# Kernel optimization log

Hardware: AMD Instinct MI355X
Metric: run time of the kernel (lower is better)

## Reference

```python
import jax, jax.numpy as jnp
import numpy as np

N, E, H, OUT, L = 50000, 500000, 256, 128, 2
EPS = 1e-5  # torch LayerNorm default


def _make_edges(k):
    # both rows cover all N nodes so that unique()/remap in the original is identity
    k1, k2, kp = jax.random.split(k, 3)
    row0 = jnp.concatenate([jax.random.permutation(kp, N), jax.random.randint(k1, (E - N,), 0, N)])
    row1 = jnp.concatenate([jnp.arange(N), jax.random.randint(k2, (E - N,), 0, N)])
    return jnp.stack([row0, row1]).astype(jnp.int32)


def setup_inputs() -> dict:
    key = jax.random.key(0)
    ks = jax.random.split(key, 7)
    s = 0.02
    x = jax.random.normal(ks[0], (N, H), jnp.float32)
    edge_r1 = _make_edges(ks[1])
    edge_r2 = _make_edges(ks[2])
    Wl = jax.random.normal(ks[3], (L, H, H), jnp.float32) * s
    W0 = jax.random.normal(ks[4], (L, H, H), jnp.float32) * s
    W1 = jax.random.normal(ks[5], (L, H, H), jnp.float32) * s
    bl = jnp.zeros((L, H), jnp.float32)
    b0 = jnp.zeros((L, H), jnp.float32)
    b1 = jnp.zeros((L, H), jnp.float32)
    gamma = jnp.ones((L, H), jnp.float32)
    beta = jnp.zeros((L, H), jnp.float32)
    Wout = jax.random.normal(ks[6], (OUT, H), jnp.float32) * s
    bout = jnp.zeros((OUT,), jnp.float32)
    return dict(x=x, edge_r1=edge_r1, edge_r2=edge_r2, Wl=Wl, bl=bl, W0=W0, b0=b0,
                W1=W1, b1=b1, gamma=gamma, beta=beta, Wout=Wout, bout=bout)


def _layer(i, h, x0, e, Wl, bl, W0, b0, W1, b1, gamma, beta):
    # PyG flow='target_to_source', aggr='add': gather h at e[1], scatter-add at e[0]
    agg = jax.ops.segment_sum(h[e[1]], e[0], num_segments=h.shape[0])  # [N, H]
    z = agg @ Wl[i].T + bl[i] + h @ W0[i].T + b0[i] + x0 @ W1[i].T + b1[i]
    z = jax.nn.relu(z)
    mu = jnp.mean(z, axis=-1, keepdims=True)
    var = jnp.mean(jnp.square(z - mu), axis=-1, keepdims=True)
    return (z - mu) * jax.lax.rsqrt(var + EPS) * gamma[i] + beta[i]  # dropout is identity in eval


def reference(x, edge_r1, edge_r2, Wl, bl, W0, b0, W1, b1, gamma, beta, Wout, bout):
    # reversed(metapath): (C,r2,C) with conv_idx=1 first, then (C,r1,C) with conv_idx=0
    h = _layer(1, x, x, edge_r2, Wl, bl, W0, b0, W1, b1, gamma, beta)
    h = _layer(0, h, x, edge_r1, Wl, bl, W0, b0, W1, b1, gamma, beta)
    return h @ Wout.T + bout  # [N, OUT]
```

## Files before the change

kernel.cpp:

```cpp
#include <hip/hip_runtime.h>
#include <stdint.h>

#define N_NODES 50000
#define N_EDGES 500000
#define NPAD    50048
#define NB      196
#define EPS     1e-5f

typedef _Float16 half8_ __attribute__((ext_vector_type(8)));
typedef _Float16 half4_ __attribute__((ext_vector_type(4)));
typedef float    float4_ __attribute__((ext_vector_type(4)));

typedef uint32_t u32_g __attribute__((address_space(1)));
typedef uint32_t u32_s __attribute__((address_space(3)));

__device__ __forceinline__ void gload16(const void* g, void* lds_wave_base) {
    __builtin_amdgcn_global_load_lds((const u32_g*)g, (u32_s*)lds_wave_base, 16, 0, 0);
}

__global__ void count_rank_kernel(const int* __restrict__ e1, const int* __restrict__ e2,
                                  int* __restrict__ cnt, int* __restrict__ ranks,
                                  int e, int n) {
    const int set = blockIdx.y;
    const int* dst = set ? e2 : e1;
    int* c = cnt + set * n;
    int* r = ranks + set * e;
    int i0 = (blockIdx.x * 256 + threadIdx.x) * 8;
    if (i0 >= e) return;
    int4 d0 = *(const int4*)(dst + i0);
    int4 d1 = *(const int4*)(dst + i0 + 4);
    int r0 = atomicAdd(&c[d0.x], 1);
    int r1 = atomicAdd(&c[d0.y], 1);
    int r2 = atomicAdd(&c[d0.z], 1);
    int r3 = atomicAdd(&c[d0.w], 1);
    int r4 = atomicAdd(&c[d1.x], 1);
    int r5 = atomicAdd(&c[d1.y], 1);
    int r6 = atomicAdd(&c[d1.z], 1);
    int r7 = atomicAdd(&c[d1.w], 1);
    *(int4*)(r + i0)     = make_int4(r0, r1, r2, r3);
    *(int4*)(r + i0 + 4) = make_int4(r4, r5, r6, r7);
}

__global__ void bsum_kernel(const int* __restrict__ cnt, int* __restrict__ bsums, int n) {
    const int* c = cnt + blockIdx.y * n;
    int i = blockIdx.x * 256 + threadIdx.x;
    int v = (i < n) ? c[i] : 0;
    for (int off = 32; off > 0; off >>= 1) v += __shfl_xor(v, off, 64);
    __shared__ int ws[4];
    if ((threadIdx.x & 63) == 0) ws[threadIdx.x >> 6] = v;
    __syncthreads();
    if (threadIdx.x == 0)
        bsums[blockIdx.y * 256 + blockIdx.x] = ws[0] + ws[1] + ws[2] + ws[3];
}

__global__ void bscan_kernel(int* __restrict__ bsums, int* __restrict__ rp1,
                             int* __restrict__ rp2, int nb, int n) {
    __shared__ int sm[512];
    int t = threadIdx.x;
    int idx = t & 255;
    int v = (idx < nb) ? bsums[t] : 0;
    sm[t] = v;
    __syncthreads();
    for (int off = 1; off < 256; off <<= 1) {
        int x = sm[t];
        if (idx >= off) x += sm[t - off];
        __syncthreads();
        sm[t] = x;
        __syncthreads();
    }
    if (idx < nb) bsums[t] = (idx > 0) ? sm[t - 1] : 0;
    if (t == 255)  rp1[n] = sm[255];
    if (t == 511)  rp2[n] = sm[511];
}

__global__ void bscatter_kernel(const int* __restrict__ cnt, const int* __restrict__ bsums,
                                int* __restrict__ rp, int n) {
    const int* c = cnt + blockIdx.y * n;
    int* rpS = rp + blockIdx.y * (n + 1);
    __shared__ int sm[256];
    int t = threadIdx.x;
    int i = blockIdx.x * 256 + t;
    int v = (i < n) ? c[i] : 0;
    sm[t] = v;
    __syncthreads();
    for (int off = 1; off < 256; off <<= 1) {
        int x = sm[t];
        if (t >= off) x += sm[t - off];
        __syncthreads();
        sm[t] = x;
        __syncthreads();
    }
    int excl = sm[t] - v + bsums[blockIdx.y * 256 + blockIdx.x];
    if (i < n) rpS[i] = excl;
}

__global__ void place_kernel(const int* __restrict__ e1, const int* __restrict__ e2,
                             const int* __restrict__ ranks, const int* __restrict__ rp,
                             int* __restrict__ col, int e, int n) {
    const int set = blockIdx.y;
    const int* ed = set ? e2 : e1;
    const int* r  = ranks + set * e;
    const int* rpS = rp + set * (n + 1);
    int* cl = col + set * e;
    int i0 = (blockIdx.x * 256 + threadIdx.x) * 8;
    if (i0 >= e) return;
    int4 d0 = *(const int4*)(ed + i0);
    int4 d1 = *(const int4*)(ed + i0 + 4);
    int4 s0 = *(const int4*)(ed + e + i0);
    int4 s1 = *(const int4*)(ed + e + i0 + 4);
    int4 k0 = *(const int4*)(r + i0);
    int4 k1 = *(const int4*)(r + i0 + 4);
    int p0 = rpS[d0.x] + k0.x;
    int p1 = rpS[d0.y] + k0.y;
    int p2 = rpS[d0.z] + k0.z;
    int p3 = rpS[d0.w] + k0.w;
    int p4 = rpS[d1.x] + k1.x;
    int p5 = rpS[d1.y] + k1.y;
    int p6 = rpS[d1.z] + k1.z;
    int p7 = rpS[d1.w] + k1.w;
    cl[p0] = s0.x; cl[p1] = s0.y; cl[p2] = s0.z; cl[p3] = s0.w;
    cl[p4] = s1.x; cl[p5] = s1.y; cl[p6] = s1.z; cl[p7] = s1.w;
}

__global__ void copyx_kernel(const float* __restrict__ x, _Float16* __restrict__ xh, int n) {
    int i = blockIdx.x * 256 + threadIdx.x;
    if (i >= n * 64) return;
    float4_ v = ((const float4_*)x)[i];
    half4_ h;
    h[0] = (_Float16)v[0]; h[1] = (_Float16)v[1];
    h[2] = (_Float16)v[2]; h[3] = (_Float16)v[3];
    ((half4_*)xh)[i] = h;
}

__global__ void pad_kernel(_Float16* __restrict__ a, _Float16* __restrict__ b,
                           _Float16* __restrict__ c, _Float16* __restrict__ d) {
    int i = blockIdx.x * 256 + threadIdx.x;
    int buf = i / 3072, j = i % 3072;
    _Float16* p = (buf == 0) ? a : (buf == 1) ? b : (buf == 2) ? c : d;
    half4_ z = {(_Float16)0.f, (_Float16)0.f, (_Float16)0.f, (_Float16)0.f};
    *(half4_*)(p + (size_t)N_NODES * 256 + (size_t)j * 4) = z;
}

__global__ void wcat_kernel(const float* __restrict__ Wl, const float* __restrict__ W0,
                            const float* __restrict__ W1, const float* __restrict__ Wout,
                            _Float16* __restrict__ Wcat) {
    int i = blockIdx.x * 256 + threadIdx.x;
    if (i < 2 * 256 * 768) {
        int l = i / (256 * 768);
        int r = i % (256 * 768);
        int j = r / 768, k = r % 768;
        const float* s = (k < 256) ? Wl : (k < 512 ? W0 : W1);
        Wcat[i] = (_Float16)s[l * 65536 + j * 256 + (k & 255)];
    } else if (i < 2 * 256 * 768 + 128 * 256) {
        int r = i - 2 * 256 * 768;
        Wcat[i] = (_Float16)Wout[r];
    }
}

__global__ void bias_kernel(const float* __restrict__ bl, const float* __restrict__ b0,
                            const float* __restrict__ b1, const float* __restrict__ bout,
                            float* __restrict__ bias) {
    int i = blockIdx.x * 256 + threadIdx.x;
    if (i < 512)       bias[i] = bl[i] + b0[i] + b1[i];
    else if (i < 640)  bias[i] = bout[i - 512];
}

__global__ void gather_kernel(const _Float16* __restrict__ hin,
                              const int* __restrict__ rowptr, const int* __restrict__ col,
                              _Float16* __restrict__ dst, int n) {
    int node = blockIdx.x * 4 + (threadIdx.x >> 6);
    int lane = threadIdx.x & 63;
    int half = lane >> 5, l5 = lane & 31;
    if (node >= n) return;
    int s = rowptr[node], e = rowptr[node + 1];
    float a[8] = {0.f, 0.f, 0.f, 0.f, 0.f, 0.f, 0.f, 0.f};
    float b[8] = {0.f, 0.f, 0.f, 0.f, 0.f, 0.f, 0.f, 0.f};
    int i = s + half;
    for (; i + 2 < e; i += 4) {
        int c0 = col[i], c1 = col[i + 2];
        half8_ v0 = *(const half8_*)(hin + (size_t)c0 * 256 + l5 * 8);
        half8_ v1 = *(const half8_*)(hin + (size_t)c1 * 256 + l5 * 8);
#pragma unroll
        for (int j = 0; j < 8; j++) { a[j] += (float)v0[j]; b[j] += (float)v1[j]; }
    }
    for (; i < e; i += 2) {
        int c0 = col[i];
        half8_ v0 = *(const half8_*)(hin + (size_t)c0 * 256 + l5 * 8);
#pragma unroll
        for (int j = 0; j < 8; j++) a[j] += (float)v0[j];
    }
    half8_ o;
#pragma unroll
    for (int j = 0; j < 8; j++) {
        float t = a[j] + b[j];
        t += __shfl_xor(t, 32, 64);
        o[j] = (_Float16)t;
    }
    if (half == 0)
        *(half8_*)(dst + (size_t)node * 256 + l5 * 8) = o;
}

__global__ __launch_bounds__(512) void gemm_ln(const _Float16* __restrict__ agg,
                                               const _Float16* __restrict__ hsrc,
                                               const _Float16* __restrict__ xh,
                                               const _Float16* __restrict__ Bw,
                                               const float* __restrict__ bias,
                                               const float* __restrict__ gamma,
                                               const float* __restrict__ beta,
                                               _Float16* __restrict__ H) {
    __shared__ __align__(16) char smem[49152];
    char* AsB = smem;
    char* BsB = smem + 16384;
    const int rowBase = blockIdx.x * 128;
    const int tid  = threadIdx.x;
    const int lane = tid & 63;
    const int w    = tid >> 6;
    const int wm = w & 1, wn = w >> 1;
    const int quad = lane >> 4, mr = lane & 15;
    const int x7 = mr & 7;

    float4_ acc[4][4];
#pragma unroll
    for (int i = 0; i < 4; i++)
#pragma unroll
        for (int j = 0; j < 4; j++) { float4_ z4 = {0.f, 0.f, 0.f, 0.f}; acc[i][j] = z4; }

    int cA0 = w * 64 + lane, cA1 = cA0 + 512;
    int rA0 = cA0 >> 3, rA1 = cA1 >> 3;
    size_t offA0 = (size_t)(rowBase + rA0) * 256 + (((cA0 & 7) ^ (rA0 & 7)) * 8);
    size_t offA1 = (size_t)(rowBase + rA1) * 256 + (((cA1 & 7) ^ (rA1 & 7)) * 8);
    size_t offB[4];
#pragma unroll
    for (int j = 0; j < 4; j++) {
        int c = j * 512 + w * 64 + lane;
        int r = c >> 3;
        offB[j] = (size_t)r * 768 + (((c & 7) ^ (r & 7)) * 8);
    }
    void* lA0 = AsB + w * 1024;
    void* lA1 = AsB + 8192 + w * 1024;

    for (int k0 = 0; k0 < 768; k0 += 64) {
        const _Float16* src = (k0 < 256) ? agg : (k0 < 512) ? hsrc : xh;
        const int kloc = k0 & 255;
        gload16(src + offA0 + kloc, lA0);
        gload16(src + offA1 + kloc, lA1);
        gload16(Bw + offB[0] + k0, BsB + w * 1024);
        gload16(Bw + offB[1] + k0, BsB + 8192 + w * 1024);
        gload16(Bw + offB[2] + k0, BsB + 16384 + w * 1024);
        gload16(Bw + offB[3] + k0, BsB + 24576 + w * 1024);
        __syncthreads();
#pragma unroll
        for (int s = 0; s < 2; s++) {
            half8_ a[4], b[4];
#pragma unroll
            for (int im = 0; im < 4; im++) {
                int row = wm * 64 + im * 16 + mr;
                a[im] = *(const half8_*)(AsB + row * 128 + (((s * 4 + quad) ^ x7) * 16));
            }
#pragma unroll
            for (int in = 0; in < 4; in++) {
                int row = wn * 64 + in * 16 + mr;
                b[in] = *(const half8_*)(BsB + row * 128 + (((s * 4 + quad) ^ x7) * 16));
            }
#pragma unroll
            for (int im = 0; im < 4; im++)
#pragma unroll
                for (int in = 0; in < 4; in++)
                    acc[im][in] = __builtin_amdgcn_mfma_f32_16x16x32_f16(a[im], b[in], acc[im][in], 0, 0, 0);
        }
        __syncthreads();
    }

    float bv[4], gv[4], bev[4];
#pragma unroll
    for (int in = 0; in < 4; in++) {
        int colg = wn * 64 + in * 16 + mr;
        bv[in]  = bias[colg];
        gv[in]  = gamma[colg];
        bev[in] = beta[colg];
    }
    float* lnbuf   = (float*)AsB;
    float* lnstats = (float*)(AsB + 4096);

#pragma unroll
    for (int im = 0; im < 4; im++)
#pragma unroll
        for (int r = 0; r < 4; r++) {
            float s = 0.f, sq = 0.f;
#pragma unroll
            for (int in = 0; in < 4; in++) {
                float v = acc[im][in][r] + bv[in];
                v = v > 0.f ? v : 0.f;
                s += v; sq += v * v;
            }
            s  += __shfl_xor(s, 1, 64);  sq += __shfl_xor(sq, 1, 64);
            s  += __shfl_xor(s, 2, 64);  sq += __shfl_xor(sq, 2, 64);
            s  += __shfl_xor(s, 4, 64);  sq += __shfl_xor(sq, 4, 64);
            s  += __shfl_xor(s, 8, 64);  sq += __shfl_xor(sq, 8, 64);
            if (mr == 0) {
                int rl = wm * 64 + im * 16 + quad * 4 + r;
                lnbuf[(wn * 128 + rl) * 2]     = s;
                lnbuf[(wn * 128 + rl) * 2 + 1] = sq;
            }
        }
    __syncthreads();
    if (tid < 128) {
        float s  = lnbuf[tid * 2]             + lnbuf[(128 + tid) * 2]
                 + lnbuf[(256 + tid) * 2]     + lnbuf[(384 + tid) * 2];
        float sq = lnbuf[tid * 2 + 1]         + lnbuf[(128 + tid) * 2 + 1]
                 + lnbuf[(256 + tid) * 2 + 1] + lnbuf[(384 + tid) * 2 + 1];
        float mu  = s * (1.0f / 256.0f);
        float var = sq * (1.0f / 256.0f) - mu * mu;
        lnstats[tid * 2]     = mu;
        lnstats[tid * 2 + 1] = rsqrtf(var + EPS);
    }
    __syncthreads();

    _Float16* BsH = (_Float16*)BsB;
#pragma unroll
    for (int p = 0; p < 2; p++) {
        if (wm == p) {
#pragma unroll
            for (int im = 0; im < 4; im++)
#pragma unroll
                for (int r = 0; r < 4; r++) {
                    int rl = im * 16 + quad * 4 + r;
                    float mu = lnstats[(p * 64 + rl) * 2];
                    float rs = lnstats[(p * 64 + rl) * 2 + 1];
#pragma unroll
                    for (int in = 0; in < 4; in++) {
                        float v = acc[im][in][r] + bv[in];
                        v = v > 0.f ? v : 0.f;
                        BsH[rl * 256 + wn * 64 + in * 16 + mr] =
                            (_Float16)((v - mu) * rs * gv[in] + bev[in]);
                    }
                }
        }
        __syncthreads();
#pragma unroll
        for (int i = 0; i < 4; i++) {
            int c = i * 512 + tid;
            int row = c >> 5, ch = c & 31;
            half8_ v = *(const half8_*)(BsB + c * 16);
            *(half8_*)(H + (size_t)(rowBase + p * 64 + row) * 256 + ch * 8) = v;
        }
        __syncthreads();
    }
}

__global__ __launch_bounds__(256) void gemm_bt(const _Float16* __restrict__ A, int lda,
                                               const _Float16* __restrict__ B, int ldb,
                                               const float* __restrict__ bias,
                                               float* __restrict__ C, int ldc,
                                               int K, int Mstore) {
    __shared__ _Float16 As[128 * 32];
    __shared__ _Float16 Bs[128 * 32];
    const int rowBase = blockIdx.x * 128;
    const int colBase = blockIdx.y * 128;
    const int tid  = threadIdx.x;
    const int lane = tid & 63;
    const int w    = tid >> 6;
    const int wm = w & 1, wn = w >> 1;
    const int quad = lane >> 4, mr = lane & 15;

    float4_ acc[4][4];
#pragma unroll
    for (int i = 0; i < 4; i++)
#pragma unroll
        for (int j = 0; j < 4; j++) { float4_ z4 = {0.f, 0.f, 0.f, 0.f}; acc[i][j] = z4; }

    const int c0  = w * 64 + lane;
    const int rA0 = c0 >> 2;
    const int ko  = (c0 & 3) * 8;
    char* AsB = (char*)As;
    char* BsB = (char*)Bs;
    void* lA0 = AsB + w * 1024;
    void* lA1 = AsB + 4096 + w * 1024;
    void* lB0 = BsB + w * 1024;
    void* lB1 = BsB + 4096 + w * 1024;
    const _Float16* gA0 = A + (size_t)(rowBase + rA0) * lda + ko;
    const _Float16* gA1 = gA0 + (size_t)64 * lda;
    const _Float16* gB0 = B + (size_t)(colBase + rA0) * ldb + ko;
    const _Float16* gB1 = gB0 + (size_t)64 * ldb;

    for (int k0 = 0; k0 < K; k0 += 32) {
        gload16(gA0 + k0, lA0);
        gload16(gA1 + k0, lA1);
        gload16(gB0 + k0, lB0);
        gload16(gB1 + k0, lB1);
        __syncthreads();
        half8_ a[4], b[4];
#pragma unroll
        for (int im = 0; im < 4; im++)
            a[im] = *(const half8_*)(AsB + ((wm * 64 + im * 16 + mr) * 64 + quad * 16));
#pragma unroll
        for (int in = 0; in < 4; in++)
            b[in] = *(const half8_*)(BsB + ((wn * 64 + in * 16 + mr) * 64 + quad * 16));
#pragma unroll
        for (int im = 0; im < 4; im++)
#pragma unroll
            for (int in = 0; in < 4; in++)
                acc[im][in] = __builtin_amdgcn_mfma_f32_16x16x32_f16(a[im], b[in], acc[im][in], 0, 0, 0);
        __syncthreads();
    }

#pragma unroll
    for (int in = 0; in < 4; in++) {
        const int colg = colBase + wn * 64 + in * 16 + mr;
        const float bv = bias[colg];
#pragma unroll
        for (int im = 0; im < 4; im++) {
            float4_ c = acc[im][in];
#pragma unroll
            for (int r = 0; r < 4; r++) {
                int row = rowBase + wm * 64 + im * 16 + quad * 4 + r;
                if (row < Mstore) C[(size_t)row * ldc + colg] = c[r] + bv;
            }
        }
    }
}

extern "C" void kernel_launch(void* const* d_in, const int* in_sizes, int n_in,
                              void* d_out, int out_size, void* d_ws, size_t ws_size,
                              hipStream_t stream) {
    const float* x    = (const float*)d_in[0];
    const int*   e1   = (const int*)d_in[1];
    const int*   e2   = (const int*)d_in[2];
    const float* Wl   = (const float*)d_in[3];
    const float* bl   = (const float*)d_in[4];
    const float* W0   = (const float*)d_in[5];
    const float* b0   = (const float*)d_in[6];
    const float* W1   = (const float*)d_in[7];
    const float* b1   = (const float*)d_in[8];
    const float* gamma= (const float*)d_in[9];
    const float* beta = (const float*)d_in[10];
    const float* Wout = (const float*)d_in[11];
    const float* bout = (const float*)d_in[12];

    char* ws = (char*)d_ws;
    size_t off = 0;
    auto alloc = [&](size_t bytes) -> char* {
        char* p = ws + off;
        off = (off + bytes + 255) & ~(size_t)255;
        return p;
    };
    _Float16* xh   = (_Float16*)alloc((size_t)NPAD * 256 * 2);
    _Float16* aggb = (_Float16*)alloc((size_t)NPAD * 256 * 2);
    _Float16* h1   = (_Float16*)alloc((size_t)NPAD * 256 * 2);
    _Float16* h2   = (_Float16*)alloc((size_t)NPAD * 256 * 2);
    _Float16* Wcat = (_Float16*)alloc((size_t)(2 * 256 * 768 + 128 * 256) * 2);
    float*    bias = (float*)alloc(640 * 4);
    int* cnt   = (int*)alloc((size_t)2 * N_NODES * 4);
    int* rp    = (int*)alloc((size_t)2 * (N_NODES + 1) * 4);
    int* ranks = (int*)alloc((size_t)2 * N_EDGES * 4);
    int* col   = (int*)alloc((size_t)2 * N_EDGES * 4);
    int* bsums = (int*)alloc(512 * 4);

    int* rp1 = rp, *rp2 = rp + (N_NODES + 1);
    int* col1 = col, *col2 = col + N_EDGES;

    hipMemsetAsync(cnt, 0, (size_t)2 * N_NODES * 4, stream);

    const int eb8 = (N_EDGES / 8 + 255) / 256;
    count_rank_kernel<<<dim3(eb8, 2), 256, 0, stream>>>(e1, e2, cnt, ranks, N_EDGES, N_NODES);
    bsum_kernel<<<dim3(NB, 2), 256, 0, stream>>>(cnt, bsums, N_NODES);
    bscan_kernel<<<1, 512, 0, stream>>>(bsums, rp1, rp2, NB, N_NODES);
    bscatter_kernel<<<dim3(NB, 2), 256, 0, stream>>>(cnt, bsums, rp, N_NODES);
    place_kernel<<<dim3(eb8, 2), 256, 0, stream>>>(e1, e2, ranks, rp, col, N_EDGES, N_NODES);

    copyx_kernel<<<12500, 256, 0, stream>>>(x, xh, N_NODES);
    pad_kernel<<<48, 256, 0, stream>>>(xh, aggb, h1, h2);
    wcat_kernel<<<(2 * 256 * 768 + 128 * 256 + 255) / 256, 256, 0, stream>>>(Wl, W0, W1, Wout, Wcat);
    bias_kernel<<<3, 256, 0, stream>>>(bl, b0, b1, bout, bias);

    const int nb4 = (N_NODES + 3) / 4;

    gather_kernel<<<nb4, 256, 0, stream>>>(xh, rp2, col2, aggb, N_NODES);
    gemm_ln<<<391, 512, 0, stream>>>(aggb, xh, xh, Wcat + 196608,
                                     bias + 256, gamma + 256, beta + 256, h1);

    gather_kernel<<<nb4, 256, 0, stream>>>(h1, rp1, col1, aggb, N_NODES);
    gemm_ln<<<391, 512, 0, stream>>>(aggb, h1, xh, Wcat,
                                     bias, gamma, beta, h2);

    gemm_bt<<<dim3(391, 1), 256, 0, stream>>>(h2, 256, Wcat + 393216, 256,
                                              bias + 512, (float*)d_out, 128, 256, N_NODES);
}
```

Before: 347.7 us.

## Merge prep kernels, use decoupled-lookback scan, fuse output GEMM into final layer

Folds the edge counting, x-to-fp16 conversion, weight concatenation, padding and bias setup into a single block-partitioned prep kernel. The three-kernel block-sum/scan/scatter sequence becomes one single-pass scan using chained lookback flags. The final output projection is fused into the second gemm_ln epilogue, reading the normalized tile from swizzled LDS, so the h2 buffer and the separate gemm_bt launch go away. This reduces launch count and an HBM round-trip of the hidden state, but the lookback scan depends on earlier blocks being scheduled first, and the fused epilogue reads Wout directly from global memory.

```diff
diff --git a/kernel.cpp b/kernel.cpp
--- a/kernel.cpp
+++ b/kernel.cpp
@@ -4,7 +4,7 @@
 #define N_NODES 50000
 #define N_EDGES 500000
 #define NPAD    50048
-#define NB      196
+#define NSCAN   196
 #define EPS     1e-5f
 
 typedef _Float16 half8_ __attribute__((ext_vector_type(8)));
@@ -18,69 +18,85 @@
     __builtin_amdgcn_global_load_lds((const u32_g*)g, (u32_s*)lds_wave_base, 16, 0, 0);
 }
 
-__global__ void count_rank_kernel(const int* __restrict__ e1, const int* __restrict__ e2,
-                                  int* __restrict__ cnt, int* __restrict__ ranks,
-                                  int e, int n) {
-    const int set = blockIdx.y;
-    const int* dst = set ? e2 : e1;
-    int* c = cnt + set * n;
-    int* r = ranks + set * e;
-    int i0 = (blockIdx.x * 256 + threadIdx.x) * 8;
-    if (i0 >= e) return;
-    int4 d0 = *(const int4*)(dst + i0);
-    int4 d1 = *(const int4*)(dst + i0 + 4);
-    int r0 = atomicAdd(&c[d0.x], 1);
-    int r1 = atomicAdd(&c[d0.y], 1);
-    int r2 = atomicAdd(&c[d0.z], 1);
-    int r3 = atomicAdd(&c[d0.w], 1);
-    int r4 = atomicAdd(&c[d1.x], 1);
-    int r5 = atomicAdd(&c[d1.y], 1);
-    int r6 = atomicAdd(&c[d1.z], 1);
-    int r7 = atomicAdd(&c[d1.w], 1);
-    *(int4*)(r + i0)     = make_int4(r0, r1, r2, r3);
-    *(int4*)(r + i0 + 4) = make_int4(r4, r5, r6, r7);
-}
-
-__global__ void bsum_kernel(const int* __restrict__ cnt, int* __restrict__ bsums, int n) {
-    const int* c = cnt + blockIdx.y * n;
-    int i = blockIdx.x * 256 + threadIdx.x;
-    int v = (i < n) ? c[i] : 0;
-    for (int off = 32; off > 0; off >>= 1) v += __shfl_xor(v, off, 64);
-    __shared__ int ws[4];
-    if ((threadIdx.x & 63) == 0) ws[threadIdx.x >> 6] = v;
-    __syncthreads();
-    if (threadIdx.x == 0)
-        bsums[blockIdx.y * 256 + blockIdx.x] = ws[0] + ws[1] + ws[2] + ws[3];
-}
-
-__global__ void bscan_kernel(int* __restrict__ bsums, int* __restrict__ rp1,
-                             int* __restrict__ rp2, int nb, int n) {
-    __shared__ int sm[512];
-    int t = threadIdx.x;
-    int idx = t & 255;
-    int v = (idx < nb) ? bsums[t] : 0;
-    sm[t] = v;
-    __syncthreads();
-    for (int off = 1; off < 256; off <<= 1) {
-        int x = sm[t];
-        if (idx >= off) x += sm[t - off];
-        __syncthreads();
-        sm[t] = x;
-        __syncthreads();
-    }
-    if (idx < nb) bsums[t] = (idx > 0) ? sm[t - 1] : 0;
-    if (t == 255)  rp1[n] = sm[255];
-    if (t == 511)  rp2[n] = sm[511];
-}
-
-__global__ void bscatter_kernel(const int* __restrict__ cnt, const int* __restrict__ bsums,
-                                int* __restrict__ rp, int n) {
-    const int* c = cnt + blockIdx.y * n;
-    int* rpS = rp + blockIdx.y * (n + 1);
+__global__ __launch_bounds__(256) void prep_kernel(
+        const int* __restrict__ e1, const int* __restrict__ e2,
+        int* __restrict__ cnt, int* __restrict__ ranks,
+        const float* __restrict__ x, _Float16* __restrict__ xh,
+        _Float16* __restrict__ aggb, _Float16* __restrict__ h1,
+        const float* __restrict__ Wl, const float* __restrict__ W0,
+        const float* __restrict__ W1, const float* __restrict__ Wout,
+        _Float16* __restrict__ Wcat,
+        const float* __restrict__ bl, const float* __restrict__ b0,
+        const float* __restrict__ b1, const float* __restrict__ bout,
+        float* __restrict__ bias) {
+    const int bid = blockIdx.x;
+    const int tid = threadIdx.x;
+    if (bid < 490) {
+        const int set = (bid >= 245);
+        const int bx  = set ? bid - 245 : bid;
+        const int* dst = set ? e2 : e1;
+        int* c = cnt + set * N_NODES;
+        int* r = ranks + set * N_EDGES;
+        int i0 = (bx * 256 + tid) * 8;
+        if (i0 >= N_EDGES) return;
+        int4 d0 = *(const int4*)(dst + i0);
+        int4 d1 = *(const int4*)(dst + i0 + 4);
+        int r0 = atomicAdd(&c[d0.x], 1);
+        int r1 = atomicAdd(&c[d0.y], 1);
+        int r2 = atomicAdd(&c[d0.z], 1);
+        int r3 = atomicAdd(&c[d0.w], 1);
+        int r4 = atomicAdd(&c[d1.x], 1);
+        int r5 = atomicAdd(&c[d1.y], 1);
+        int r6 = atomicAdd(&c[d1.z], 1);
+        int r7 = atomicAdd(&c[d1.w], 1);
+        *(int4*)(r + i0)     = make_int4(r0, r1, r2, r3);
+        *(int4*)(r + i0 + 4) = make_int4(r4, r5, r6, r7);
+    } else if (bid < 12990) {
+        int i = (bid - 490) * 256 + tid;
+        float4_ v = ((const float4_*)x)[i];
+        half4_ h;
+        h[0] = (_Float16)v[0]; h[1] = (_Float16)v[1];
+        h[2] = (_Float16)v[2]; h[3] = (_Float16)v[3];
+        ((half4_*)xh)[i] = h;
+    } else if (bid < 14654) {
+        int i = (bid - 12990) * 256 + tid;
+        if (i < 2 * 256 * 768) {
+            int l = i / (256 * 768);
+            int r = i % (256 * 768);
+            int j = r / 768, k = r % 768;
+            const float* s = (k < 256) ? Wl : (k < 512 ? W0 : W1);
+            Wcat[i] = (_Float16)s[l * 65536 + j * 256 + (k & 255)];
+        } else {
+            Wcat[i] = (_Float16)Wout[i - 2 * 256 * 768];
+        }
+    } else if (bid < 14690) {
+        int j = (bid - 14654) * 256 + tid;
+        int buf = j / 3072, jj = j % 3072;
+        _Float16* p = (buf == 0) ? xh : (buf == 1) ? aggb : h1;
+        half4_ z = {(_Float16)0.f, (_Float16)0.f, (_Float16)0.f, (_Float16)0.f};
+        *(half4_*)(p + (size_t)N_NODES * 256 + (size_t)jj * 4) = z;
+    } else {
+        int i = (bid - 14690) * 256 + tid;
+        if (i < 512)      bias[i] = bl[i] + b0[i] + b1[i];
+        else if (i < 640) bias[i] = bout[i - 512];
+    }
+}
+
+__global__ __launch_bounds__(256) void scan_kernel(const int* __restrict__ cnt,
+                                                   unsigned long long* __restrict__ state,
+                                                   int* __restrict__ rp) {
     __shared__ int sm[256];
-    int t = threadIdx.x;
-    int i = blockIdx.x * 256 + t;
-    int v = (i < n) ? c[i] : 0;
+    __shared__ int s_excl;
+    const int bid = blockIdx.x;
+    const int set = bid / NSCAN;
+    const int seq = bid % NSCAN;
+    const int t = threadIdx.x;
+    const int i = seq * 256 + t;
+    const int* c = cnt + set * N_NODES;
+    int* rpS = rp + set * (N_NODES + 1);
+    unsigned long long* st = state + set * NSCAN;
+
+    int v = (i < N_NODES) ? c[i] : 0;
     sm[t] = v;
     __syncthreads();
     for (int off = 1; off < 256; off <<= 1) {
@@ -90,8 +106,32 @@
         sm[t] = x;
         __syncthreads();
     }
-    int excl = sm[t] - v + bsums[blockIdx.y * 256 + blockIdx.x];
-    if (i < n) rpS[i] = excl;
+    int total = sm[255];
+
+    if (t == 0) {
+        if (seq == 0) {
+            atomicExch(&st[0], (2ULL << 32) | (unsigned int)total);
+            s_excl = 0;
+        } else {
+            atomicExch(&st[seq], (1ULL << 32) | (unsigned int)total);
+            int running = 0;
+            int j = seq - 1;
+            while (true) {
+                unsigned long long s = atomicAdd(&st[j], 0ULL);
+                unsigned int tag = (unsigned int)(s >> 32);
+                if (tag == 0) continue;
+                running += (int)(unsigned int)s;
+                if (tag == 2) break;
+                j--;
+            }
+            atomicExch(&st[seq], (2ULL << 32) | (unsigned int)(running + total));
+            s_excl = running;
+        }
+    }
+    __syncthreads();
+    int excl = s_excl;
+    if (i < N_NODES) rpS[i] = sm[t] - v + excl;
+    if (seq == NSCAN - 1 && t == 0) rpS[N_NODES] = excl + total;
 }
 
 __global__ void place_kernel(const int* __restrict__ e1, const int* __restrict__ e2,
@@ -122,49 +162,6 @@
     cl[p4] = s1.x; cl[p5] = s1.y; cl[p6] = s1.z; cl[p7] = s1.w;
 }
 
-__global__ void copyx_kernel(const float* __restrict__ x, _Float16* __restrict__ xh, int n) {
-    int i = blockIdx.x * 256 + threadIdx.x;
-    if (i >= n * 64) return;
-    float4_ v = ((const float4_*)x)[i];
-    half4_ h;
-    h[0] = (_Float16)v[0]; h[1] = (_Float16)v[1];
-    h[2] = (_Float16)v[2]; h[3] = (_Float16)v[3];
-    ((half4_*)xh)[i] = h;
-}
-
-__global__ void pad_kernel(_Float16* __restrict__ a, _Float16* __restrict__ b,
-                           _Float16* __restrict__ c, _Float16* __restrict__ d) {
-    int i = blockIdx.x * 256 + threadIdx.x;
-    int buf = i / 3072, j = i % 3072;
-    _Float16* p = (buf == 0) ? a : (buf == 1) ? b : (buf == 2) ? c : d;
-    half4_ z = {(_Float16)0.f, (_Float16)0.f, (_Float16)0.f, (_Float16)0.f};
-    *(half4_*)(p + (size_t)N_NODES * 256 + (size_t)j * 4) = z;
-}
-
-__global__ void wcat_kernel(const float* __restrict__ Wl, const float* __restrict__ W0,
-                            const float* __restrict__ W1, const float* __restrict__ Wout,
-                            _Float16* __restrict__ Wcat) {
-    int i = blockIdx.x * 256 + threadIdx.x;
-    if (i < 2 * 256 * 768) {
-        int l = i / (256 * 768);
-        int r = i % (256 * 768);
-        int j = r / 768, k = r % 768;
-        const float* s = (k < 256) ? Wl : (k < 512 ? W0 : W1);
-        Wcat[i] = (_Float16)s[l * 65536 + j * 256 + (k & 255)];
-    } else if (i < 2 * 256 * 768 + 128 * 256) {
-        int r = i - 2 * 256 * 768;
-        Wcat[i] = (_Float16)Wout[r];
-    }
-}
-
-__global__ void bias_kernel(const float* __restrict__ bl, const float* __restrict__ b0,
-                            const float* __restrict__ b1, const float* __restrict__ bout,
-                            float* __restrict__ bias) {
-    int i = blockIdx.x * 256 + threadIdx.x;
-    if (i < 512)       bias[i] = bl[i] + b0[i] + b1[i];
-    else if (i < 640)  bias[i] = bout[i - 512];
-}
-
 __global__ void gather_kernel(const _Float16* __restrict__ hin,
                               const int* __restrict__ rowptr, const int* __restrict__ col,
                               _Float16* __restrict__ dst, int n) {
@@ -200,6 +197,7 @@
         *(half8_*)(dst + (size_t)node * 256 + l5 * 8) = o;
 }
 
+template <bool OUTFUSE>
 __global__ __launch_bounds__(512) void gemm_ln(const _Float16* __restrict__ agg,
                                                const _Float16* __restrict__ hsrc,
                                                const _Float16* __restrict__ xh,
@@ -207,7 +205,10 @@
                                                const float* __restrict__ bias,
                                                const float* __restrict__ gamma,
                                                const float* __restrict__ beta,
-                                               _Float16* __restrict__ H) {
+                                               _Float16* __restrict__ H,
+                                               const _Float16* __restrict__ WoutH,
+                                               const float* __restrict__ biasOut,
+                                               float* __restrict__ Out) {
     __shared__ __align__(16) char smem[49152];
     char* AsB = smem;
     char* BsB = smem + 16384;
@@ -316,6 +317,13 @@
     }
     __syncthreads();
 
+    float bvo[4];
+    if (OUTFUSE) {
+#pragma unroll
+        for (int ct = 0; ct < 4; ct++)
+            bvo[ct] = biasOut[(w >> 2) * 64 + ct * 16 + mr];
+    }
+
     _Float16* BsH = (_Float16*)BsB;
 #pragma unroll
     for (int p = 0; p < 2; p++) {
@@ -331,92 +339,51 @@
                     for (int in = 0; in < 4; in++) {
                         float v = acc[im][in][r] + bv[in];
                         v = v > 0.f ? v : 0.f;
-                        BsH[rl * 256 + wn * 64 + in * 16 + mr] =
-                            (_Float16)((v - mu) * rs * gv[in] + bev[in]);
+                        int colg = wn * 64 + in * 16 + mr;
+                        int off2 = rl * 256 + (((colg >> 3) ^ (rl & 31)) << 3) + (colg & 7);
+                        BsH[off2] = (_Float16)((v - mu) * rs * gv[in] + bev[in]);
                     }
                 }
         }
         __syncthreads();
-#pragma unroll
-        for (int i = 0; i < 4; i++) {
-            int c = i * 512 + tid;
-            int row = c >> 5, ch = c & 31;
-            half8_ v = *(const half8_*)(BsB + c * 16);
-            *(half8_*)(H + (size_t)(rowBase + p * 64 + row) * 256 + ch * 8) = v;
-        }
-        __syncthreads();
-    }
-}
-
-__global__ __launch_bounds__(256) void gemm_bt(const _Float16* __restrict__ A, int lda,
-                                               const _Float16* __restrict__ B, int ldb,
-                                               const float* __restrict__ bias,
-                                               float* __restrict__ C, int ldc,
-                                               int K, int Mstore) {
-    __shared__ _Float16 As[128 * 32];
-    __shared__ _Float16 Bs[128 * 32];
-    const int rowBase = blockIdx.x * 128;
-    const int colBase = blockIdx.y * 128;
-    const int tid  = threadIdx.x;
-    const int lane = tid & 63;
-    const int w    = tid >> 6;
-    const int wm = w & 1, wn = w >> 1;
-    const int quad = lane >> 4, mr = lane & 15;
-
-    float4_ acc[4][4];
-#pragma unroll
-    for (int i = 0; i < 4; i++)
-#pragma unroll
-        for (int j = 0; j < 4; j++) { float4_ z4 = {0.f, 0.f, 0.f, 0.f}; acc[i][j] = z4; }
-
-    const int c0  = w * 64 + lane;
-    const int rA0 = c0 >> 2;
-    const int ko  = (c0 & 3) * 8;
-    char* AsB = (char*)As;
-    char* BsB = (char*)Bs;
-    void* lA0 = AsB + w * 1024;
-    void* lA1 = AsB + 4096 + w * 1024;
-    void* lB0 = BsB + w * 1024;
-    void* lB1 = BsB + 4096 + w * 1024;
-    const _Float16* gA0 = A + (size_t)(rowBase + rA0) * lda + ko;
-    const _Float16* gA1 = gA0 + (size_t)64 * lda;
-    const _Float16* gB0 = B + (size_t)(colBase + rA0) * ldb + ko;
-    const _Float16* gB1 = gB0 + (size_t)64 * ldb;
-
-    for (int k0 = 0; k0 < K; k0 += 32) {
-        gload16(gA0 + k0, lA0);
-        gload16(gA1 + k0, lA1);
-        gload16(gB0 + k0, lB0);
-        gload16(gB1 + k0, lB1);
-        __syncthreads();
-        half8_ a[4], b[4];
-#pragma unroll
-        for (int im = 0; im < 4; im++)
-            a[im] = *(const half8_*)(AsB + ((wm * 64 + im * 16 + mr) * 64 + quad * 16));
-#pragma unroll
-        for (int in = 0; in < 4; in++)
-            b[in] = *(const half8_*)(BsB + ((wn * 64 + in * 16 + mr) * 64 + quad * 16));
-#pragma unroll
-        for (int im = 0; im < 4; im++)
-#pragma unroll
-            for (int in = 0; in < 4; in++)
-                acc[im][in] = __builtin_amdgcn_mfma_f32_16x16x32_f16(a[im], b[in], acc[im][in], 0, 0, 0);
-        __syncthreads();
-    }
-
-#pragma unroll
-    for (int in = 0; in < 4; in++) {
-        const int colg = colBase + wn * 64 + in * 16 + mr;
-        const float bv = bias[colg];
-#pragma unroll
-        for (int im = 0; im < 4; im++) {
-            float4_ c = acc[im][in];
-#pragma unroll
-            for (int r = 0; r < 4; r++) {
-                int row = rowBase + wm * 64 + im * 16 + quad * 4 + r;
-                if (row < Mstore) C[(size_t)row * ldc + colg] = c[r] + bv;
-            }
-        }
+        if (!OUTFUSE) {
+#pragma unroll
+            for (int i = 0; i < 4; i++) {
+                int c = i * 512 + tid;
+                int row = c >> 5, ch = c & 31;
+                half8_ v = *(const half8_*)(BsB + row * 512 + ((ch ^ (row & 31)) << 4));
+                *(half8_*)(H + (size_t)(rowBase + p * 64 + row) * 256 + ch * 8) = v;
+            }
+        } else {
+            const int rt = w & 3;
+            const int chh = w >> 2;
+            float4_ acc2[4];
+#pragma unroll
+            for (int ct = 0; ct < 4; ct++) { float4_ z4 = {0.f, 0.f, 0.f, 0.f}; acc2[ct] = z4; }
+            const int rA = rt * 16 + mr;
+#pragma unroll
+            for (int s2 = 0; s2 < 8; s2++) {
+                int ck = s2 * 4 + quad;
+                half8_ a2 = *(const half8_*)(BsB + rA * 512 + ((ck ^ (rA & 31)) << 4));
+#pragma unroll
+                for (int ct = 0; ct < 4; ct++) {
+                    int colg = chh * 64 + ct * 16 + mr;
+                    half8_ b2 = *(const half8_*)(WoutH + (size_t)colg * 256 + s2 * 32 + quad * 8);
+                    acc2[ct] = __builtin_amdgcn_mfma_f32_16x16x32_f16(a2, b2, acc2[ct], 0, 0, 0);
+                }
+            }
+#pragma unroll
+            for (int ct = 0; ct < 4; ct++) {
+                int colg = chh * 64 + ct * 16 + mr;
+#pragma unroll
+                for (int r = 0; r < 4; r++) {
+                    int row = rowBase + p * 64 + rt * 16 + quad * 4 + r;
+                    if (row < N_NODES)
+                        Out[(size_t)row * 128 + colg] = acc2[ct][r] + bvo[ct];
+                }
+            }
+        }
+        __syncthreads();
     }
 }
 
@@ -447,42 +414,36 @@
     _Float16* xh   = (_Float16*)alloc((size_t)NPAD * 256 * 2);
     _Float16* aggb = (_Float16*)alloc((size_t)NPAD * 256 * 2);
     _Float16* h1   = (_Float16*)alloc((size_t)NPAD * 256 * 2);
-    _Float16* h2   = (_Float16*)alloc((size_t)NPAD * 256 * 2);
     _Float16* Wcat = (_Float16*)alloc((size_t)(2 * 256 * 768 + 128 * 256) * 2);
     float*    bias = (float*)alloc(640 * 4);
     int* cnt   = (int*)alloc((size_t)2 * N_NODES * 4);
+    unsigned long long* states = (unsigned long long*)alloc((size_t)2 * NSCAN * 8);
     int* rp    = (int*)alloc((size_t)2 * (N_NODES + 1) * 4);
     int* ranks = (int*)alloc((size_t)2 * N_EDGES * 4);
     int* col   = (int*)alloc((size_t)2 * N_EDGES * 4);
-    int* bsums = (int*)alloc(512 * 4);
 
     int* rp1 = rp, *rp2 = rp + (N_NODES + 1);
     int* col1 = col, *col2 = col + N_EDGES;
 
-    hipMemsetAsync(cnt, 0, (size_t)2 * N_NODES * 4, stream);
-
+    size_t zbytes = (size_t)((char*)states + 2 * NSCAN * 8 - (char*)cnt);
+    hipMemsetAsync(cnt, 0, zbytes, stream);
+
+    prep_kernel<<<14693, 256, 0, stream>>>(e1, e2, cnt, ranks, x, xh, aggb, h1,
+                                           Wl, W0, W1, Wout, Wcat,
+                                           bl, b0, b1, bout, bias);
+    scan_kernel<<<2 * NSCAN, 256, 0, stream>>>(cnt, states, rp);
     const int eb8 = (N_EDGES / 8 + 255) / 256;
-    count_rank_kernel<<<dim3(eb8, 2), 256, 0, stream>>>(e1, e2, cnt, ranks, N_EDGES, N_NODES);
-    bsum_kernel<<<dim3(NB, 2), 256, 0, stream>>>(cnt, bsums, N_NODES);
-    bscan_kernel<<<1, 512, 0, stream>>>(bsums, rp1, rp2, NB, N_NODES);
-    bscatter_kernel<<<dim3(NB, 2), 256, 0, stream>>>(cnt, bsums, rp, N_NODES);
     place_kernel<<<dim3(eb8, 2), 256, 0, stream>>>(e1, e2, ranks, rp, col, N_EDGES, N_NODES);
 
-    copyx_kernel<<<12500, 256, 0, stream>>>(x, xh, N_NODES);
-    pad_kernel<<<48, 256, 0, stream>>>(xh, aggb, h1, h2);
-    wcat_kernel<<<(2 * 256 * 768 + 128 * 256 + 255) / 256, 256, 0, stream>>>(Wl, W0, W1, Wout, Wcat);
-    bias_kernel<<<3, 256, 0, stream>>>(bl, b0, b1, bout, bias);
-
     const int nb4 = (N_NODES + 3) / 4;
+    const _Float16* WoutH = Wcat + 393216;
 
     gather_kernel<<<nb4, 256, 0, stream>>>(xh, rp2, col2, aggb, N_NODES);
-    gemm_ln<<<391, 512, 0, stream>>>(aggb, xh, xh, Wcat + 196608,
-                                     bias + 256, gamma + 256, beta + 256, h1);
-
+    gemm_ln<false><<<391, 512, 0, stream>>>(aggb, xh, xh, Wcat + 196608,
+                                            bias + 256, gamma + 256, beta + 256, h1,
+                                            nullptr, nullptr, nullptr);
     gather_kernel<<<nb4, 256, 0, stream>>>(h1, rp1, col1, aggb, N_NODES);
-    gemm_ln<<<391, 512, 0, stream>>>(aggb, h1, xh, Wcat,
-                                     bias, gamma, beta, h2);
-
-    gemm_bt<<<dim3(391, 1), 256, 0, stream>>>(h2, 256, Wcat + 393216, 256,
-                                              bias + 512, (float*)d_out, 128, 256, N_NODES);
-}
+    gemm_ln<true><<<391, 512, 0, stream>>>(aggb, h1, xh, Wcat,
+                                           bias, gamma, beta, nullptr,
+                                           WoutH, bias + 512, (float*)d_out);
+}
```

After: 370.9 us. +6.7%, slower.
